# Performance work log

Measured on AMD Instinct MI355X. Metric: run time of the kernel, lower is better.

The kernel has to match this reference:

```python
import jax, jax.numpy as jnp
import numpy as np

N = 100000      # nodes
E = 1600000     # directed edges
F_IN = 128      # num_node_features
H = 256         # hidden_dim
OUT = 128       # output_dim
G = 2048        # number of graphs in batch
EPS = 1e-5      # BatchNorm eps


def setup_inputs() -> dict:
    key = jax.random.key(0)
    ks = jax.random.split(key, 8)
    x = jax.random.normal(ks[0], (N, F_IN), jnp.float32)
    row = jax.random.randint(ks[1], (E,), 0, N, dtype=jnp.int32)
    col = jax.random.randint(ks[2], (E,), 0, N, dtype=jnp.int32)
    batch = jnp.sort(jax.random.randint(ks[3], (N,), 0, G, dtype=jnp.int32))

    def lin(k, fi, fo):
        return (jax.random.normal(k, (fi, fo), jnp.float32) / np.sqrt(fi)).astype(jnp.float32)

    return {
        "x": x, "row": row, "col": col, "batch": batch,
        "W1": lin(ks[4], F_IN, H), "b1": jnp.zeros((H,), jnp.float32),
        "g1": jnp.ones((H,), jnp.float32), "be1": jnp.zeros((H,), jnp.float32),
        "W2": lin(ks[5], H, H), "b2": jnp.zeros((H,), jnp.float32),
        "g2": jnp.ones((H,), jnp.float32), "be2": jnp.zeros((H,), jnp.float32),
        "W3": lin(ks[6], H, OUT), "b3": jnp.zeros((OUT,), jnp.float32),
        "g3": jnp.ones((OUT,), jnp.float32), "be3": jnp.zeros((OUT,), jnp.float32),
    }


def gcn_conv(x, W, b, row, col):
    # PyG GCNConv: add self-loops, symmetric deg normalization, then scatter-add.
    h = x @ W                                              # [N, F_out]
    deg = jnp.ones((N,), x.dtype).at[col].add(jnp.ones((E,), x.dtype))  # +1 for self-loop
    dinv = jax.lax.rsqrt(deg)                              # deg >= 1, safe
    norm = dinv[row] * dinv[col]                           # [E]
    agg = jnp.zeros_like(h).at[col].add(h[row] * norm[:, None])
    agg = agg + h * (dinv * dinv)[:, None]                 # self-loop messages
    return agg + b


def batchnorm(x, g, b):
    # training-mode batch statistics (running stats at init are 0/1 anyway)
    m = x.mean(axis=0)
    v = x.var(axis=0)
    return g * (x - m) * jax.lax.rsqrt(v + EPS) + b


def reference(x, row, col, batch, W1, b1, g1, be1, W2, b2, g2, be2, W3, b3, g3, be3):
    h = jax.nn.relu(batchnorm(gcn_conv(x, W1, b1, row, col), g1, be1))
    h = jax.nn.relu(batchnorm(gcn_conv(h, W2, b2, row, col), g2, be2))
    h = batchnorm(gcn_conv(h, W3, b3, row, col), g3, be3)
    # global_mean_pool over graphs
    sums = jax.ops.segment_sum(h, batch, num_segments=G)   # [G, OUT]
    cnt = jax.ops.segment_sum(jnp.ones((N,), h.dtype), batch, num_segments=G)
    return sums / jnp.maximum(cnt, 1.0)[:, None]
```

## Files before the change

### kernel.cpp

```cpp
#include <hip/hip_runtime.h>

#define NN 100000
#define EE 1600000
#define GG 2048
#define EPSB 1e-5f
#define MP 100096
#define MBLK (MP / 128)
#define NB 782
#define CAP 2560

typedef unsigned short u16;
typedef unsigned long long u64;
typedef __attribute__((ext_vector_type(8))) short short8;
typedef __attribute__((ext_vector_type(4))) float f32x4;

struct alignas(4)  u16x2 { u16 v[2]; };
struct alignas(8)  u16x4 { u16 v[4]; };
struct alignas(16) u16x8 { u16 v[8]; };

__device__ __forceinline__ float b2f(u16 u) { return __uint_as_float(((unsigned)u) << 16); }
__device__ __forceinline__ u16 f2b(float f) {
    unsigned u = __float_as_uint(f);
    return (u16)((u + 0x7FFF + ((u >> 16) & 1)) >> 16);
}
__device__ __forceinline__ void gload16(const void* g, void* l) {
    __builtin_amdgcn_global_load_lds((const __attribute__((address_space(1))) void*)g,
                                     (__attribute__((address_space(3))) void*)l, 16, 0, 0);
}


__global__ void bucketA_kernel(const int* __restrict__ row, const int* __restrict__ col,
                               int* __restrict__ bcur, u64* __restrict__ bkt) {
    int e = blockIdx.x * 256 + threadIdx.x;
    if (e < EE) {
        int c = col[e], r = row[e];
        int b = c >> 7;
        int p = atomicAdd(&bcur[b * 16], 1);
        if (p < CAP) bkt[(size_t)b * CAP + p] = ((u64)r << 32) | (unsigned)c;
    }
}

__global__ void bucketB_kernel(const u64* __restrict__ bkt, const int* __restrict__ bcur,
                               int* __restrict__ pfx, int* __restrict__ rcnt,
                               float* __restrict__ dinv, int* __restrict__ btot) {
    int b = blockIdx.x, t = threadIdx.x;
    __shared__ int lcnt[128];
    __shared__ int sp[128];
    if (t < 128) lcnt[t] = 0;
    __syncthreads();
    int tot = bcur[b * 16];
    if (tot > CAP) tot = CAP;
    const u64* B = bkt + (size_t)b * CAP;
    for (int i = t; i < tot; i += 256) atomicAdd(&lcnt[(int)(B[i] & 127)], 1);
    __syncthreads();
    int n0 = b << 7;
    int pc = 0;
    if (t < 128) {
        int c = lcnt[t];
        if (n0 + t < NN) dinv[n0 + t] = rsqrtf((float)(c + 1));
        rcnt[b * 128 + t] = c;
        pc = (c + 7) & ~7;
        sp[t] = pc;
    }
    __syncthreads();
    for (int o = 1; o < 128; o <<= 1) {
        int u = (t >= o && t < 128) ? sp[t - o] : 0;
        __syncthreads();
        if (t < 128) sp[t] += u;
        __syncthreads();
    }
    if (t < 128) pfx[b * 128 + t] = sp[t] - pc;
    if (t == 127) btot[b] = sp[127];
}

__global__ void scanT_kernel(int* __restrict__ btot, float* __restrict__ dinv,
                             int* __restrict__ colptr) {
    __shared__ int sh[1024];
    int t = threadIdx.x;
    int v = (t < NB) ? btot[t] : 0;
    sh[t] = v;
    __syncthreads();
    for (int o = 1; o < 1024; o <<= 1) {
        int u = (t >= o) ? sh[t - o] : 0;
        __syncthreads();
        sh[t] += u;
        __syncthreads();
    }
    if (t < NB) btot[t] = sh[t] - v;
    if (t == NB - 1) colptr[NN] = sh[t];
    if (t == 0) dinv[NN] = 0.f;
}

__global__ void bucketC_kernel(const u64* __restrict__ bkt, const int* __restrict__ bcur,
                               const int* __restrict__ pfx, const int* __restrict__ rcnt,
                               const int* __restrict__ btot, int* __restrict__ colptr,
                               int* __restrict__ srcs) {
    int b = blockIdx.x, t = threadIdx.x;
    int n0 = b << 7;
    __shared__ int cur[128];
    int base = btot[b];
    if (t < 128) {
        int st = base + pfx[b * 128 + t];
        cur[t] = st;
        if (n0 + t < NN) colptr[n0 + t] = st;
    }
    __syncthreads();
    int tot = bcur[b * 16];
    if (tot > CAP) tot = CAP;
    const u64* B = bkt + (size_t)b * CAP;
    for (int i = t; i < tot; i += 256) {
        u64 v = B[i];
        int c = (int)(v & 127);
        int r = (int)(v >> 32);
        int p = atomicAdd(&cur[c], 1);
        srcs[p] = r;
    }
    __syncthreads();
    if (t < 128) {
        int rc = rcnt[b * 128 + t];
        int pc = (rc + 7) & ~7;
        int st = base + pfx[b * 128 + t];
        for (int i = rc; i < pc; ++i) srcs[st + i] = NN;
    }
}


__global__ void xcast_kernel(const float* __restrict__ x, u16* __restrict__ xb) {
    int idx = blockIdx.x * 256 + threadIdx.x;
    if (idx < NN * 32) {
        float4 v = ((const float4*)x)[idx];
        u16x4 o = {{f2b(v.x), f2b(v.y), f2b(v.z), f2b(v.w)}};
        ((u16x4*)xb)[idx] = o;
    }
}

__global__ void wcast_kernel(const float* __restrict__ W1, const float* __restrict__ W2,
                             const float* __restrict__ W3, u16* __restrict__ Wt1,
                             u16* __restrict__ Wt2, u16* __restrict__ Wt3) {
    int idx = blockIdx.x * 256 + threadIdx.x;
    if (idx < 32768) {
        int n = idx >> 7, k = idx & 127;
        Wt1[idx] = f2b(W1[k * 256 + n]);
    } else if (idx < 98304) {
        int j = idx - 32768;
        int n = j >> 8, k = j & 255;
        Wt2[j] = f2b(W2[k * 256 + n]);
    } else if (idx < 131072) {
        int j = idx - 98304;
        int n = j >> 8, k = j & 255;
        Wt3[j] = f2b(W3[k * 128 + n]);
    }
}


template <int F, bool TR>
__global__ void agg_kernel(const u16* __restrict__ X, u16* __restrict__ out,
                           const int* __restrict__ colptr, const int* __restrict__ srcs,
                           const float* __restrict__ dinv,
                           const float* __restrict__ sc, const float* __restrict__ shf) {
    constexpr int VE = F / 64;
    int node = blockIdx.x * 4 + (threadIdx.x >> 6);
    if (node >= NN) return;
    int l = threadIdx.x & 63;
    int f0 = l * VE;
    float s_[VE], t_[VE];
    if (TR) {
#pragma unroll
        for (int j = 0; j < VE; ++j) { s_[j] = sc[f0 + j]; t_[j] = shf[f0 + j]; }
    }
    float acc[VE] = {};
    int beg = colptr[node], end = colptr[node + 1];

    auto fetch = [&](int s, u16* u) {
        if (VE == 4) *(u16x4*)u = *(const u16x4*)(X + (size_t)s * F + f0);
        else         *(u16x2*)u = *(const u16x2*)(X + (size_t)s * F + f0);
    };
    auto accum = [&](const u16* u, float w) {
#pragma unroll
        for (int j = 0; j < VE; ++j) {
            float v = b2f(u[j]);
            if (TR) v = fmaxf(fmaf(s_[j], v, t_[j]), 0.f);
            acc[j] = fmaf(w, v, acc[j]);
        }
    };

    for (int e0 = beg; e0 < end; e0 += 64) {
        int take = end - e0;
        if (take > 64) take = 64;
        int sv = (l < take) ? srcs[e0 + l] : NN;
        float wv = dinv[sv];
        for (int j = 0; j < take; j += 8) {
            int s[8];
            float w[8];
            u16 u[8][VE];
#pragma unroll
            for (int q = 0; q < 8; ++q) {
                s[q] = __shfl(sv, j + q);
                w[q] = __shfl(wv, j + q);
            }
#pragma unroll
            for (int q = 0; q < 8; ++q) fetch(s[q], u[q]);
#pragma unroll
            for (int q = 0; q < 8; ++q) accum(u[q], w[q]);
        }
    }
    float di = dinv[node];
    u16 us[VE];
    fetch(node, us);
    accum(us, di);
    if (VE == 4) {
        u16x4 o = {{f2b(di * acc[0]), f2b(di * acc[1]), f2b(di * acc[2]), f2b(di * acc[3])}};
        *(u16x4*)(out + (size_t)node * F + f0) = o;
    } else {
        u16x2 o = {{f2b(di * acc[0]), f2b(di * acc[1])}};
        *(u16x2*)(out + (size_t)node * F + f0) = o;
    }
}


template <bool STATS, bool FUSEA>
__global__ __launch_bounds__(256) void gemm_kernel(const u16* __restrict__ A,
                                                   const u16* __restrict__ Wt,
                                                   u16* __restrict__ C,
                                                   int Kdim, int Nout,
                                                   float* __restrict__ gs,
                                                   const float* __restrict__ sc,
                                                   const float* __restrict__ shf) {
    __shared__ u16 As[128 * 64];
    __shared__ u16 Bs[128 * 64];
    __shared__ float sbuf[2][128];
    const int tid = threadIdx.x;
    const int w = tid >> 6, l = tid & 63;
    const int row0 = blockIdx.x * 128;
    const int col0 = blockIdx.y * 128;
    const int srow = w * 32 + (l >> 3);
    const int skel = (l & 7) * 8;
    const u16* Asrc = A + (size_t)(row0 + srow) * Kdim + skel;
    const u16* Bsrc = Wt + (size_t)(col0 + srow) * Kdim + skel;
    u16* AsBase = &As[w * 2048];
    u16* BsBase = &Bs[w * 2048];
    const int wr = (w >> 1) * 64, wc = (w & 1) * 64;
    f32x4 acc[4][4] = {};
    if (STATS && tid < 128) { sbuf[0][tid] = 0.f; sbuf[1][tid] = 0.f; }

    for (int k0 = 0; k0 < Kdim; k0 += 64) {
        if (FUSEA) {
            float4 sa0 = *(const float4*)&sc[k0 + skel];
            float4 sa1 = *(const float4*)&sc[k0 + skel + 4];
            float4 ta0 = *(const float4*)&shf[k0 + skel];
            float4 ta1 = *(const float4*)&shf[k0 + skel + 4];
            float sA[8] = {sa0.x, sa0.y, sa0.z, sa0.w, sa1.x, sa1.y, sa1.z, sa1.w};
            float tA[8] = {ta0.x, ta0.y, ta0.z, ta0.w, ta1.x, ta1.y, ta1.z, ta1.w};
#pragma unroll
            for (int j = 0; j < 4; ++j) {
                u16x8 av = *(const u16x8*)(Asrc + (size_t)(j * 8) * Kdim + k0);
                u16x8 o;
#pragma unroll
                for (int i = 0; i < 8; ++i)
                    o.v[i] = f2b(fmaxf(fmaf(sA[i], b2f(av.v[i]), tA[i]), 0.f));
                *(u16x8*)&As[(w * 32 + j * 8 + (l >> 3)) * 64 + skel] = o;
            }
        } else {
#pragma unroll
            for (int j = 0; j < 4; ++j)
                gload16(Asrc + (size_t)(j * 8) * Kdim + k0, AsBase + j * 512);
        }
#pragma unroll
        for (int j = 0; j < 4; ++j)
            gload16(Bsrc + (size_t)(j * 8) * Kdim + k0, BsBase + j * 512);
        __syncthreads();
#pragma unroll
        for (int ks = 0; ks < 2; ++ks) {
            short8 a[4], b[4];
#pragma unroll
            for (int mi = 0; mi < 4; ++mi)
                a[mi] = *(const short8*)&As[(wr + mi * 16 + (l & 15)) * 64 + ks * 32 + (l >> 4) * 8];
#pragma unroll
            for (int ni = 0; ni < 4; ++ni)
                b[ni] = *(const short8*)&Bs[(wc + ni * 16 + (l & 15)) * 64 + ks * 32 + (l >> 4) * 8];
#pragma unroll
            for (int mi = 0; mi < 4; ++mi)
#pragma unroll
                for (int ni = 0; ni < 4; ++ni)
                    acc[mi][ni] = __builtin_amdgcn_mfma_f32_16x16x32_bf16(a[mi], b[ni], acc[mi][ni], 0, 0, 0);
        }
        __syncthreads();
    }
    const int cr = (l >> 4) * 4, cc = l & 15;
#pragma unroll
    for (int mi = 0; mi < 4; ++mi) {
#pragma unroll
        for (int j = 0; j < 4; ++j) {
            int r = row0 + wr + mi * 16 + cr + j;
#pragma unroll
            for (int ni = 0; ni < 4; ++ni)
                C[(size_t)r * Nout + col0 + wc + ni * 16 + cc] = f2b(acc[mi][ni][j]);
        }
    }
    if (STATS) {
#pragma unroll
        for (int ni = 0; ni < 4; ++ni) {
            float s = 0.f, q = 0.f;
#pragma unroll
            for (int mi = 0; mi < 4; ++mi)
#pragma unroll
                for (int jj = 0; jj < 4; ++jj) {
                    float v = acc[mi][ni][jj];
                    s += v;
                    q += v * v;
                }
            s += __shfl_xor(s, 16); s += __shfl_xor(s, 32);
            q += __shfl_xor(q, 16); q += __shfl_xor(q, 32);
            if (l < 16) {
                atomicAdd(&sbuf[0][wc + ni * 16 + l], s);
                atomicAdd(&sbuf[1][wc + ni * 16 + l], q);
            }
        }
        __syncthreads();
        if (tid < 128) {
            size_t base = (size_t)(blockIdx.y * gridDim.x + blockIdx.x) * 256;
            gs[base + tid] = sbuf[0][tid];
            gs[base + 128 + tid] = sbuf[1][tid];
        }
    }
}

__global__ void statreduce_kernel(const float* __restrict__ gs, float* __restrict__ sums, int F) {
    int which = blockIdx.x;
    int by = blockIdx.y;
    int c = threadIdx.x;
    float s = 0.f;
    for (int bx = 0; bx < MBLK; ++bx)
        s += gs[(size_t)(by * MBLK + bx) * 256 + which * 128 + c];
    sums[which * F + by * 128 + c] = s;
}


__global__ void stats_kernel(const u16* __restrict__ Z, int F, float* __restrict__ sums) {
    int f = threadIdx.x;
    float s = 0.f, q = 0.f;
    for (int r = blockIdx.x; r < NN; r += gridDim.x) {
        float v = b2f(Z[(size_t)r * F + f]);
        s += v;
        q += v * v;
    }
    atomicAdd(&sums[f], s);
    atomicAdd(&sums[F + f], q);
}

__global__ void finalize_kernel(const float* __restrict__ sums, int F,
                                const float* __restrict__ g, const float* __restrict__ be,
                                float* __restrict__ sc, float* __restrict__ shf) {
    int f = threadIdx.x;
    if (f < F) {
        float m = sums[f] * (1.f / NN);
        float v = sums[F + f] * (1.f / NN) - m * m;
        float s = g[f] * rsqrtf(v + EPSB);
        sc[f] = s;
        shf[f] = be[f] - m * s;
    }
}


__global__ void pool_kernel(const u16* __restrict__ Z, const int* __restrict__ batch,
                            const float* __restrict__ sc, const float* __restrict__ shf,
                            float* __restrict__ out) {
    int gph = blockIdx.x;
    int f = threadIdx.x;
    __shared__ int sb, se;
    if (f == 0) {
        int lo = 0, hi = NN;
        while (lo < hi) { int mid = (lo + hi) >> 1; if (batch[mid] < gph) lo = mid + 1; else hi = mid; }
        sb = lo;
        hi = NN;
        while (lo < hi) { int mid = (lo + hi) >> 1; if (batch[mid] < gph + 1) lo = mid + 1; else hi = mid; }
        se = lo;
    }
    __syncthreads();
    int beg = sb, end = se;
    float acc = 0.f;
    for (int r = beg; r < end; ++r) acc += b2f(Z[(size_t)r * 128 + f]);
    float res = 0.f;
    int c = end - beg;
    if (c > 0) res = fmaf(sc[f], acc / (float)c, shf[f]);
    out[(size_t)gph * 128 + f] = res;
}


extern "C" void kernel_launch(void* const* d_in, const int* in_sizes, int n_in,
                              void* d_out, int out_size, void* d_ws, size_t ws_size,
                              hipStream_t stream) {
    const float* x     = (const float*)d_in[0];
    const int*   row   = (const int*)d_in[1];
    const int*   col   = (const int*)d_in[2];
    const int*   batch = (const int*)d_in[3];
    const float* W1 = (const float*)d_in[4];
    const float* g1 = (const float*)d_in[6];
    const float* be1 = (const float*)d_in[7];
    const float* W2 = (const float*)d_in[8];
    const float* g2 = (const float*)d_in[10];
    const float* be2 = (const float*)d_in[11];
    const float* W3 = (const float*)d_in[12];
    const float* g3 = (const float*)d_in[14];
    const float* be3 = (const float*)d_in[15];
    float* out = (float*)d_out;

    char* ws = (char*)d_ws;
    size_t off = 0;
    auto alloc = [&](size_t bytes) { size_t o = off; off += (bytes + 255) & ~255ULL; return o; };
    u16*   bufA   = (u16*)  (ws + alloc((size_t)MP * 256 * 2));
    u16*   bufB   = (u16*)  (ws + alloc((size_t)MP * 256 * 2));
    u16*   xb     = (u16*)  (ws + alloc((size_t)MP * 128 * 2));
    u16*   Wt1    = (u16*)  (ws + alloc(128 * 256 * 2));
    u16*   Wt2    = (u16*)  (ws + alloc(256 * 256 * 2));
    u16*   Wt3    = (u16*)  (ws + alloc(256 * 128 * 2));
    int*   colptr = (int*)  (ws + alloc((size_t)(NN + 16) * 4));
    float* dinv   = (float*)(ws + alloc((size_t)(NN + 16) * 4));
    int*   srcs   = (int*)  (ws + alloc((size_t)(EE + 8 * NN) * 4));
    u64*   bkt    = (u64*)  (ws + alloc((size_t)NB * CAP * 8));
    int*   bcur   = (int*)  (ws + alloc((size_t)NB * 16 * 4));
    int*   pfx    = (int*)  (ws + alloc((size_t)NB * 128 * 4));
    int*   rcnt   = (int*)  (ws + alloc((size_t)NB * 128 * 4));
    int*   btot   = (int*)  (ws + alloc(1024 * 4));
    float* stats  = (float*)(ws + alloc(6 * 256 * 4));
    float* scbuf  = (float*)(ws + alloc(6 * 256 * 4));
    float* gs     = (float*)(ws + alloc((size_t)MBLK * 2 * 256 * 4));

    hipMemsetAsync(bcur, 0, (size_t)NB * 16 * 4, stream);
    hipMemsetAsync(stats, 0, 6 * 256 * 4, stream);
    hipMemsetAsync((char*)bufA + (size_t)NN * 256, 0, (size_t)(MP - NN) * 256, stream);
    hipMemsetAsync((char*)bufA + (size_t)NN * 512, 0, (size_t)(MP - NN) * 512, stream);
    hipMemsetAsync((char*)xb + (size_t)NN * 256, 0, (size_t)(MP - NN) * 256, stream);

    bucketA_kernel<<<(EE + 255) / 256, 256, 0, stream>>>(row, col, bcur, bkt);
    bucketB_kernel<<<NB, 256, 0, stream>>>(bkt, bcur, pfx, rcnt, dinv, btot);
    scanT_kernel<<<1, 1024, 0, stream>>>(btot, dinv, colptr);
    bucketC_kernel<<<NB, 256, 0, stream>>>(bkt, bcur, pfx, rcnt, btot, colptr, srcs);

    xcast_kernel<<<(NN * 32 + 255) / 256, 256, 0, stream>>>(x, xb);
    wcast_kernel<<<512, 256, 0, stream>>>(W1, W2, W3, Wt1, Wt2, Wt3);

    const int aggBlocks = (NN + 3) / 4;

    agg_kernel<128, false><<<aggBlocks, 256, 0, stream>>>(xb, bufA, colptr, srcs, dinv, nullptr, nullptr);
    gemm_kernel<true, false><<<dim3(MBLK, 2), 256, 0, stream>>>(bufA, Wt1, bufB, 128, 256, gs, nullptr, nullptr);
    statreduce_kernel<<<dim3(2, 2), 128, 0, stream>>>(gs, stats + 0, 256);
    finalize_kernel<<<1, 256, 0, stream>>>(stats + 0, 256, g1, be1, scbuf + 0, scbuf + 256);

    agg_kernel<256, true><<<aggBlocks, 256, 0, stream>>>(bufB, bufA, colptr, srcs, dinv, scbuf + 0, scbuf + 256);
    gemm_kernel<true, false><<<dim3(MBLK, 2), 256, 0, stream>>>(bufA, Wt2, bufB, 256, 256, gs, nullptr, nullptr);
    statreduce_kernel<<<dim3(2, 2), 128, 0, stream>>>(gs, stats + 512, 256);
    finalize_kernel<<<1, 256, 0, stream>>>(stats + 512, 256, g2, be2, scbuf + 512, scbuf + 768);

    gemm_kernel<false, true><<<dim3(MBLK, 1), 256, 0, stream>>>(bufB, Wt3, bufA, 256, 128, gs, scbuf + 512, scbuf + 768);
    agg_kernel<128, false><<<aggBlocks, 256, 0, stream>>>(bufA, xb, colptr, srcs, dinv, nullptr, nullptr);
    stats_kernel<<<512, 128, 0, stream>>>(xb, 128, stats + 1024);
    finalize_kernel<<<1, 256, 0, stream>>>(stats + 1024, 128, g3, be3, scbuf + 1024, scbuf + 1280);

    pool_kernel<<<GG, 128, 0, stream>>>(xb, batch, scbuf + 1024, scbuf + 1280, out);
}
```

Measured before the change: 611.4 us.

## Repack aggregation to 16-byte lanes, pack edge buckets, fuse BN stats into pooling

The aggregation kernel now gives each lane 8 bf16 features, loaded as one 16-byte access, and uses subwave groups of 16 or 32 lanes per node. Gathers are double-buffered so the next batch of neighbour rows is fetched while the current one accumulates. Edge buckets pack source and local column into a 32-bit word instead of 64 bits, halving bucket traffic. The separate final BatchNorm stats pass is folded into a pooling pass that also writes per-graph sums, and a small kernel applies the affine transform afterwards. The packing assumes the source index fits in 25 bits, and gathers that are not multiples of 8 rely on the padded sentinel entries.

```diff
diff --git a/kernel.cpp b/kernel.cpp
--- a/kernel.cpp
+++ b/kernel.cpp
@@ -10,9 +10,9 @@
 #define CAP 2560
 
 typedef unsigned short u16;
-typedef unsigned long long u64;
 typedef __attribute__((ext_vector_type(8))) short short8;
 typedef __attribute__((ext_vector_type(4))) float f32x4;
+typedef __attribute__((ext_vector_type(2))) float f32x2;
 
 struct alignas(4)  u16x2 { u16 v[2]; };
 struct alignas(8)  u16x4 { u16 v[4]; };
@@ -30,17 +30,17 @@
 
 
 __global__ void bucketA_kernel(const int* __restrict__ row, const int* __restrict__ col,
-                               int* __restrict__ bcur, u64* __restrict__ bkt) {
+                               int* __restrict__ bcur, unsigned* __restrict__ bkt) {
     int e = blockIdx.x * 256 + threadIdx.x;
     if (e < EE) {
         int c = col[e], r = row[e];
         int b = c >> 7;
         int p = atomicAdd(&bcur[b * 16], 1);
-        if (p < CAP) bkt[(size_t)b * CAP + p] = ((u64)r << 32) | (unsigned)c;
-    }
-}
-
-__global__ void bucketB_kernel(const u64* __restrict__ bkt, const int* __restrict__ bcur,
+        if (p < CAP) bkt[(size_t)b * CAP + p] = ((unsigned)r << 7) | (unsigned)(c & 127);
+    }
+}
+
+__global__ void bucketB_kernel(const unsigned* __restrict__ bkt, const int* __restrict__ bcur,
                                int* __restrict__ pfx, int* __restrict__ rcnt,
                                float* __restrict__ dinv, int* __restrict__ btot) {
     int b = blockIdx.x, t = threadIdx.x;
@@ -50,8 +50,8 @@
     __syncthreads();
     int tot = bcur[b * 16];
     if (tot > CAP) tot = CAP;
-    const u64* B = bkt + (size_t)b * CAP;
-    for (int i = t; i < tot; i += 256) atomicAdd(&lcnt[(int)(B[i] & 127)], 1);
+    const unsigned* B = bkt + (size_t)b * CAP;
+    for (int i = t; i < tot; i += 256) atomicAdd(&lcnt[(int)(B[i] & 127u)], 1);
     __syncthreads();
     int n0 = b << 7;
     int pc = 0;
@@ -91,7 +91,7 @@
     if (t == 0) dinv[NN] = 0.f;
 }
 
-__global__ void bucketC_kernel(const u64* __restrict__ bkt, const int* __restrict__ bcur,
+__global__ void bucketC_kernel(const unsigned* __restrict__ bkt, const int* __restrict__ bcur,
                                const int* __restrict__ pfx, const int* __restrict__ rcnt,
                                const int* __restrict__ btot, int* __restrict__ colptr,
                                int* __restrict__ srcs) {
@@ -107,11 +107,11 @@
     __syncthreads();
     int tot = bcur[b * 16];
     if (tot > CAP) tot = CAP;
-    const u64* B = bkt + (size_t)b * CAP;
+    const unsigned* B = bkt + (size_t)b * CAP;
     for (int i = t; i < tot; i += 256) {
-        u64 v = B[i];
-        int c = (int)(v & 127);
-        int r = (int)(v >> 32);
+        unsigned v = B[i];
+        int c = (int)(v & 127u);
+        int r = (int)(v >> 7);
         int p = atomicAdd(&cur[c], 1);
         srcs[p] = r;
     }
@@ -153,68 +153,86 @@
 }
 
 
-template <int F, bool TR>
+template <int XS, bool TR>
 __global__ void agg_kernel(const u16* __restrict__ X, u16* __restrict__ out,
                            const int* __restrict__ colptr, const int* __restrict__ srcs,
                            const float* __restrict__ dinv,
                            const float* __restrict__ sc, const float* __restrict__ shf) {
-    constexpr int VE = F / 64;
-    int node = blockIdx.x * 4 + (threadIdx.x >> 6);
+    constexpr int GROUP = XS / 8;
+    constexpr int NPB = 256 / GROUP;
+    int node = blockIdx.x * NPB + threadIdx.x / GROUP;
     if (node >= NN) return;
-    int l = threadIdx.x & 63;
-    int f0 = l * VE;
-    float s_[VE], t_[VE];
+    int l = threadIdx.x & (GROUP - 1);
+    int f0 = l * 8;
+    const u16* Xf = X + f0;
+    f32x2 s2[4], t2[4];
     if (TR) {
-#pragma unroll
-        for (int j = 0; j < VE; ++j) { s_[j] = sc[f0 + j]; t_[j] = shf[f0 + j]; }
-    }
-    float acc[VE] = {};
+        float4 sa = *(const float4*)&sc[f0], sb = *(const float4*)&sc[f0 + 4];
+        float4 ta = *(const float4*)&shf[f0], tb = *(const float4*)&shf[f0 + 4];
+        s2[0] = f32x2{sa.x, sa.y}; s2[1] = f32x2{sa.z, sa.w};
+        s2[2] = f32x2{sb.x, sb.y}; s2[3] = f32x2{sb.z, sb.w};
+        t2[0] = f32x2{ta.x, ta.y}; t2[1] = f32x2{ta.z, ta.w};
+        t2[2] = f32x2{tb.x, tb.y}; t2[3] = f32x2{tb.z, tb.w};
+    }
+    f32x2 acc[4] = {};
+    const f32x2 z2 = {0.f, 0.f};
+
+    auto accum = [&](const u16x8& u, float w) {
+        f32x2 w2 = {w, w};
+        const unsigned* p = (const unsigned*)&u;
+#pragma unroll
+        for (int j = 0; j < 4; ++j) {
+            unsigned q = p[j];
+            f32x2 v = {__uint_as_float(q << 16), __uint_as_float(q & 0xffff0000u)};
+            if (TR) {
+                v = __builtin_elementwise_fma(s2[j], v, t2[j]);
+                v = __builtin_elementwise_max(v, z2);
+            }
+            acc[j] = __builtin_elementwise_fma(w2, v, acc[j]);
+        }
+    };
+
+#define FETCHB(kk, buf) do { _Pragma("unroll") \
+    for (int q = 0; q < 8; ++q) { \
+        int s_ = __shfl(sv, (kk) * 8 + q, GROUP); \
+        buf[q] = *(const u16x8*)(Xf + (size_t)s_ * XS); } } while (0)
+#define ACCB(kk, buf) do { _Pragma("unroll") \
+    for (int q = 0; q < 8; ++q) { \
+        float w_ = __shfl(wv, (kk) * 8 + q, GROUP); \
+        accum(buf[q], w_); } } while (0)
+
     int beg = colptr[node], end = colptr[node + 1];
-
-    auto fetch = [&](int s, u16* u) {
-        if (VE == 4) *(u16x4*)u = *(const u16x4*)(X + (size_t)s * F + f0);
-        else         *(u16x2*)u = *(const u16x2*)(X + (size_t)s * F + f0);
-    };
-    auto accum = [&](const u16* u, float w) {
-#pragma unroll
-        for (int j = 0; j < VE; ++j) {
-            float v = b2f(u[j]);
-            if (TR) v = fmaxf(fmaf(s_[j], v, t_[j]), 0.f);
-            acc[j] = fmaf(w, v, acc[j]);
-        }
-    };
-
-    for (int e0 = beg; e0 < end; e0 += 64) {
+    for (int e0 = beg; e0 < end; e0 += GROUP) {
         int take = end - e0;
-        if (take > 64) take = 64;
+        if (take > GROUP) take = GROUP;
         int sv = (l < take) ? srcs[e0 + l] : NN;
         float wv = dinv[sv];
-        for (int j = 0; j < take; j += 8) {
-            int s[8];
-            float w[8];
-            u16 u[8][VE];
-#pragma unroll
-            for (int q = 0; q < 8; ++q) {
-                s[q] = __shfl(sv, j + q);
-                w[q] = __shfl(wv, j + q);
-            }
-#pragma unroll
-            for (int q = 0; q < 8; ++q) fetch(s[q], u[q]);
-#pragma unroll
-            for (int q = 0; q < 8; ++q) accum(u[q], w[q]);
-        }
-    }
+        int b = take >> 3;
+        u16x8 A_[8], B_[8];
+        FETCHB(0, A_);
+        int k = 1;
+        for (; k + 1 < b; k += 2) {
+            FETCHB(k, B_); ACCB(k - 1, A_);
+            FETCHB(k + 1, A_); ACCB(k, B_);
+        }
+        if (k < b) { FETCHB(k, B_); ACCB(k - 1, A_); ACCB(k, B_); }
+        else ACCB(k - 1, A_);
+    }
+#undef FETCHB
+#undef ACCB
+
     float di = dinv[node];
-    u16 us[VE];
-    fetch(node, us);
+    u16x8 us = *(const u16x8*)(Xf + (size_t)node * XS);
     accum(us, di);
-    if (VE == 4) {
-        u16x4 o = {{f2b(di * acc[0]), f2b(di * acc[1]), f2b(di * acc[2]), f2b(di * acc[3])}};
-        *(u16x4*)(out + (size_t)node * F + f0) = o;
-    } else {
-        u16x2 o = {{f2b(di * acc[0]), f2b(di * acc[1])}};
-        *(u16x2*)(out + (size_t)node * F + f0) = o;
-    }
+    f32x2 d2 = {di, di};
+    u16x8 o;
+#pragma unroll
+    for (int j = 0; j < 4; ++j) {
+        f32x2 r = acc[j] * d2;
+        o.v[2 * j] = f2b(r[0]);
+        o.v[2 * j + 1] = f2b(r[1]);
+    }
+    *(u16x8*)(out + (size_t)node * XS + f0) = o;
 }
 
 
@@ -335,19 +353,6 @@
     sums[which * F + by * 128 + c] = s;
 }
 
-
-__global__ void stats_kernel(const u16* __restrict__ Z, int F, float* __restrict__ sums) {
-    int f = threadIdx.x;
-    float s = 0.f, q = 0.f;
-    for (int r = blockIdx.x; r < NN; r += gridDim.x) {
-        float v = b2f(Z[(size_t)r * F + f]);
-        s += v;
-        q += v * v;
-    }
-    atomicAdd(&sums[f], s);
-    atomicAdd(&sums[F + f], q);
-}
-
 __global__ void finalize_kernel(const float* __restrict__ sums, int F,
                                 const float* __restrict__ g, const float* __restrict__ be,
                                 float* __restrict__ sc, float* __restrict__ shf) {
@@ -362,9 +367,9 @@
 }
 
 
-__global__ void pool_kernel(const u16* __restrict__ Z, const int* __restrict__ batch,
-                            const float* __restrict__ sc, const float* __restrict__ shf,
-                            float* __restrict__ out) {
+__global__ void poolstats_kernel(const u16* __restrict__ Z, const int* __restrict__ batch,
+                                 float* __restrict__ gsum, int* __restrict__ gcnt,
+                                 float* __restrict__ sums) {
     int gph = blockIdx.x;
     int f = threadIdx.x;
     __shared__ int sb, se;
@@ -378,12 +383,27 @@
     }
     __syncthreads();
     int beg = sb, end = se;
-    float acc = 0.f;
-    for (int r = beg; r < end; ++r) acc += b2f(Z[(size_t)r * 128 + f]);
-    float res = 0.f;
-    int c = end - beg;
-    if (c > 0) res = fmaf(sc[f], acc / (float)c, shf[f]);
-    out[(size_t)gph * 128 + f] = res;
+    float acc = 0.f, qq = 0.f;
+    for (int r = beg; r < end; ++r) {
+        float v = b2f(Z[(size_t)r * 128 + f]);
+        acc += v;
+        qq += v * v;
+    }
+    gsum[(size_t)gph * 128 + f] = acc;
+    if (f == 0) gcnt[gph] = end - beg;
+    atomicAdd(&sums[f], acc);
+    atomicAdd(&sums[128 + f], qq);
+}
+
+__global__ void poolout_kernel(const float* __restrict__ gsum, const int* __restrict__ gcnt,
+                               const float* __restrict__ sc, const float* __restrict__ shf,
+                               float* __restrict__ out) {
+    int i = blockIdx.x * 256 + threadIdx.x;
+    if (i < GG * 128) {
+        int g = i >> 7, f = i & 127;
+        int c = gcnt[g];
+        out[i] = (c > 0) ? fmaf(sc[f], gsum[i] / (float)c, shf[f]) : 0.f;
+    }
 }
 
 
@@ -417,7 +437,7 @@
     int*   colptr = (int*)  (ws + alloc((size_t)(NN + 16) * 4));
     float* dinv   = (float*)(ws + alloc((size_t)(NN + 16) * 4));
     int*   srcs   = (int*)  (ws + alloc((size_t)(EE + 8 * NN) * 4));
-    u64*   bkt    = (u64*)  (ws + alloc((size_t)NB * CAP * 8));
+    unsigned* bkt = (unsigned*)(ws + alloc((size_t)NB * CAP * 4));
     int*   bcur   = (int*)  (ws + alloc((size_t)NB * 16 * 4));
     int*   pfx    = (int*)  (ws + alloc((size_t)NB * 128 * 4));
     int*   rcnt   = (int*)  (ws + alloc((size_t)NB * 128 * 4));
@@ -425,6 +445,8 @@
     float* stats  = (float*)(ws + alloc(6 * 256 * 4));
     float* scbuf  = (float*)(ws + alloc(6 * 256 * 4));
     float* gs     = (float*)(ws + alloc((size_t)MBLK * 2 * 256 * 4));
+    float* gsum   = (float*)(ws + alloc((size_t)GG * 128 * 4));
+    int*   gcnt   = (int*)  (ws + alloc((size_t)GG * 4));
 
     hipMemsetAsync(bcur, 0, (size_t)NB * 16 * 4, stream);
     hipMemsetAsync(stats, 0, 6 * 256 * 4, stream);
@@ -440,22 +462,19 @@
     xcast_kernel<<<(NN * 32 + 255) / 256, 256, 0, stream>>>(x, xb);
     wcast_kernel<<<512, 256, 0, stream>>>(W1, W2, W3, Wt1, Wt2, Wt3);
 
-    const int aggBlocks = (NN + 3) / 4;
-
-    agg_kernel<128, false><<<aggBlocks, 256, 0, stream>>>(xb, bufA, colptr, srcs, dinv, nullptr, nullptr);
+    agg_kernel<128, false><<<NN / 16, 256, 0, stream>>>(xb, bufA, colptr, srcs, dinv, nullptr, nullptr);
     gemm_kernel<true, false><<<dim3(MBLK, 2), 256, 0, stream>>>(bufA, Wt1, bufB, 128, 256, gs, nullptr, nullptr);
     statreduce_kernel<<<dim3(2, 2), 128, 0, stream>>>(gs, stats + 0, 256);
     finalize_kernel<<<1, 256, 0, stream>>>(stats + 0, 256, g1, be1, scbuf + 0, scbuf + 256);
 
-    agg_kernel<256, true><<<aggBlocks, 256, 0, stream>>>(bufB, bufA, colptr, srcs, dinv, scbuf + 0, scbuf + 256);
+    agg_kernel<256, true><<<NN / 8, 256, 0, stream>>>(bufB, bufA, colptr, srcs, dinv, scbuf + 0, scbuf + 256);
     gemm_kernel<true, false><<<dim3(MBLK, 2), 256, 0, stream>>>(bufA, Wt2, bufB, 256, 256, gs, nullptr, nullptr);
     statreduce_kernel<<<dim3(2, 2), 128, 0, stream>>>(gs, stats + 512, 256);
     finalize_kernel<<<1, 256, 0, stream>>>(stats + 512, 256, g2, be2, scbuf + 512, scbuf + 768);
 
     gemm_kernel<false, true><<<dim3(MBLK, 1), 256, 0, stream>>>(bufB, Wt3, bufA, 256, 128, gs, scbuf + 512, scbuf + 768);
-    agg_kernel<128, false><<<aggBlocks, 256, 0, stream>>>(bufA, xb, colptr, srcs, dinv, nullptr, nullptr);
-    stats_kernel<<<512, 128, 0, stream>>>(xb, 128, stats + 1024);
+    agg_kernel<128, false><<<NN / 16, 256, 0, stream>>>(bufA, xb, colptr, srcs, dinv, nullptr, nullptr);
+    poolstats_kernel<<<GG, 128, 0, stream>>>(xb, batch, gsum, gcnt, stats + 1024);
     finalize_kernel<<<1, 256, 0, stream>>>(stats + 1024, 128, g3, be3, scbuf + 1024, scbuf + 1280);
-
-    pool_kernel<<<GG, 128, 0, stream>>>(xb, batch, scbuf + 1024, scbuf + 1280, out);
-}
+    poolout_kernel<<<(GG * 128 + 255) / 256, 256, 0, stream>>>(gsum, gcnt, scbuf + 1024, scbuf + 1280, out);
+}
```

Result: slower. 807.0 us (+32.0%).

## Fuse setup kernels, drop global scan, merge stats into pooling pass

Applied to the files above, without the earlier changes.

Replaces the memsets with one init kernel and merges the bucket count and scatter kernels. It drops the global prefix scan by giving each bucket a fixed CAPP slot with per-node begin and end arrays. Bucket entries are packed into 32 bits, and the x and W cast kernels are fused. It folds the layer-3 statistics pass into the pooling read and fuses statreduce with finalize. The goal is fewer launches and one less full pass over the final activations, at the cost of a sparser srcs layout and a fixed per-bucket capacity assumption.

```diff
diff --git a/kernel.cpp b/kernel.cpp
--- a/kernel.cpp
+++ b/kernel.cpp
@@ -8,9 +8,9 @@
 #define MBLK (MP / 128)
 #define NB 782
 #define CAP 2560
+#define CAPP 3584
 
 typedef unsigned short u16;
-typedef unsigned long long u64;
 typedef __attribute__((ext_vector_type(8))) short short8;
 typedef __attribute__((ext_vector_type(4))) float f32x4;
 
@@ -29,37 +29,55 @@
 }
 
 
+#define ZB0 (NB * 16)
+#define ZB1 (ZB0 + 256)
+#define ZB2 (ZB1 + 1)
+#define ZB3 (ZB2 + (MP - NN) * 64)
+#define ZB4 (ZB3 + (MP - NN) * 128)
+
+__global__ void init_kernel(unsigned* __restrict__ bcur, unsigned* __restrict__ p3stats,
+                            unsigned* __restrict__ dinvNN, unsigned* __restrict__ padA128,
+                            unsigned* __restrict__ padA256) {
+    int i = blockIdx.x * 256 + threadIdx.x;
+    if (i < ZB0) bcur[i] = 0u;
+    else if (i < ZB1) p3stats[i - ZB0] = 0u;
+    else if (i < ZB2) dinvNN[0] = 0u;
+    else if (i < ZB3) padA128[i - ZB2] = 0u;
+    else if (i < ZB4) padA256[i - ZB3] = 0u;
+}
+
+
 __global__ void bucketA_kernel(const int* __restrict__ row, const int* __restrict__ col,
-                               int* __restrict__ bcur, u64* __restrict__ bkt) {
+                               int* __restrict__ bcur, unsigned* __restrict__ bkt) {
     int e = blockIdx.x * 256 + threadIdx.x;
     if (e < EE) {
         int c = col[e], r = row[e];
         int b = c >> 7;
         int p = atomicAdd(&bcur[b * 16], 1);
-        if (p < CAP) bkt[(size_t)b * CAP + p] = ((u64)r << 32) | (unsigned)c;
-    }
-}
-
-__global__ void bucketB_kernel(const u64* __restrict__ bkt, const int* __restrict__ bcur,
-                               int* __restrict__ pfx, int* __restrict__ rcnt,
-                               float* __restrict__ dinv, int* __restrict__ btot) {
+        if (p < CAP) bkt[(size_t)b * CAP + p] = ((unsigned)r << 7) | (unsigned)(c & 127);
+    }
+}
+
+__global__ void bucketBC_kernel(const unsigned* __restrict__ bkt, const int* __restrict__ bcur,
+                                int* __restrict__ begs, int* __restrict__ ends,
+                                float* __restrict__ dinv, int* __restrict__ srcs) {
     int b = blockIdx.x, t = threadIdx.x;
     __shared__ int lcnt[128];
     __shared__ int sp[128];
+    __shared__ int cur[128];
     if (t < 128) lcnt[t] = 0;
     __syncthreads();
     int tot = bcur[b * 16];
     if (tot > CAP) tot = CAP;
-    const u64* B = bkt + (size_t)b * CAP;
-    for (int i = t; i < tot; i += 256) atomicAdd(&lcnt[(int)(B[i] & 127)], 1);
+    const unsigned* B = bkt + (size_t)b * CAP;
+    for (int i = t; i < tot; i += 256) atomicAdd(&lcnt[(int)(B[i] & 127u)], 1);
     __syncthreads();
     int n0 = b << 7;
     int pc = 0;
     if (t < 128) {
-        int c = lcnt[t];
-        if (n0 + t < NN) dinv[n0 + t] = rsqrtf((float)(c + 1));
-        rcnt[b * 128 + t] = c;
-        pc = (c + 7) & ~7;
+        int rc = lcnt[t];
+        if (n0 + t < NN) dinv[n0 + t] = rsqrtf((float)(rc + 1));
+        pc = (rc + 7) & ~7;
         sp[t] = pc;
     }
     __syncthreads();
@@ -69,94 +87,58 @@
         if (t < 128) sp[t] += u;
         __syncthreads();
     }
-    if (t < 128) pfx[b * 128 + t] = sp[t] - pc;
-    if (t == 127) btot[b] = sp[127];
-}
-
-__global__ void scanT_kernel(int* __restrict__ btot, float* __restrict__ dinv,
-                             int* __restrict__ colptr) {
-    __shared__ int sh[1024];
-    int t = threadIdx.x;
-    int v = (t < NB) ? btot[t] : 0;
-    sh[t] = v;
-    __syncthreads();
-    for (int o = 1; o < 1024; o <<= 1) {
-        int u = (t >= o) ? sh[t - o] : 0;
-        __syncthreads();
-        sh[t] += u;
-        __syncthreads();
-    }
-    if (t < NB) btot[t] = sh[t] - v;
-    if (t == NB - 1) colptr[NN] = sh[t];
-    if (t == 0) dinv[NN] = 0.f;
-}
-
-__global__ void bucketC_kernel(const u64* __restrict__ bkt, const int* __restrict__ bcur,
-                               const int* __restrict__ pfx, const int* __restrict__ rcnt,
-                               const int* __restrict__ btot, int* __restrict__ colptr,
-                               int* __restrict__ srcs) {
-    int b = blockIdx.x, t = threadIdx.x;
-    int n0 = b << 7;
-    __shared__ int cur[128];
-    int base = btot[b];
+    int base = b * CAPP;
     if (t < 128) {
-        int st = base + pfx[b * 128 + t];
+        int st = base + sp[t] - pc;
         cur[t] = st;
-        if (n0 + t < NN) colptr[n0 + t] = st;
-    }
-    __syncthreads();
-    int tot = bcur[b * 16];
-    if (tot > CAP) tot = CAP;
-    const u64* B = bkt + (size_t)b * CAP;
+        if (n0 + t < NN) { begs[n0 + t] = st; ends[n0 + t] = st + pc; }
+    }
+    __syncthreads();
     for (int i = t; i < tot; i += 256) {
-        u64 v = B[i];
-        int c = (int)(v & 127);
-        int r = (int)(v >> 32);
-        int p = atomicAdd(&cur[c], 1);
-        srcs[p] = r;
-    }
-    __syncthreads();
-    if (t < 128) {
-        int rc = rcnt[b * 128 + t];
-        int pc = (rc + 7) & ~7;
-        int st = base + pfx[b * 128 + t];
-        for (int i = rc; i < pc; ++i) srcs[st + i] = NN;
-    }
-}
-
-
-__global__ void xcast_kernel(const float* __restrict__ x, u16* __restrict__ xb) {
+        unsigned v = B[i];
+        int p = atomicAdd(&cur[(int)(v & 127u)], 1);
+        srcs[p] = (int)(v >> 7);
+    }
+    __syncthreads();
+    if (t < 128 && n0 + t < NN) {
+        int st = cur[t];
+        int en = base + sp[t];
+        for (int i = st; i < en; ++i) srcs[i] = NN;
+    }
+}
+
+
+__global__ void xwcast_kernel(const float* __restrict__ x, u16* __restrict__ xb,
+                              const float* __restrict__ W1, const float* __restrict__ W2,
+                              const float* __restrict__ W3, u16* __restrict__ Wt1,
+                              u16* __restrict__ Wt2, u16* __restrict__ Wt3) {
     int idx = blockIdx.x * 256 + threadIdx.x;
     if (idx < NN * 32) {
         float4 v = ((const float4*)x)[idx];
         u16x4 o = {{f2b(v.x), f2b(v.y), f2b(v.z), f2b(v.w)}};
         ((u16x4*)xb)[idx] = o;
-    }
-}
-
-__global__ void wcast_kernel(const float* __restrict__ W1, const float* __restrict__ W2,
-                             const float* __restrict__ W3, u16* __restrict__ Wt1,
-                             u16* __restrict__ Wt2, u16* __restrict__ Wt3) {
-    int idx = blockIdx.x * 256 + threadIdx.x;
-    if (idx < 32768) {
-        int n = idx >> 7, k = idx & 127;
-        Wt1[idx] = f2b(W1[k * 256 + n]);
-    } else if (idx < 98304) {
-        int j = idx - 32768;
-        int n = j >> 8, k = j & 255;
-        Wt2[j] = f2b(W2[k * 256 + n]);
-    } else if (idx < 131072) {
-        int j = idx - 98304;
-        int n = j >> 8, k = j & 255;
-        Wt3[j] = f2b(W3[k * 128 + n]);
+        return;
+    }
+    int j = idx - NN * 32;
+    if (j < 32768) {
+        int n = j >> 7, k = j & 127;
+        Wt1[j] = f2b(W1[k * 256 + n]);
+    } else if (j < 98304) {
+        int jj = j - 32768;
+        int n = jj >> 8, k = jj & 255;
+        Wt2[jj] = f2b(W2[k * 256 + n]);
+    } else if (j < 131072) {
+        int jj = j - 98304;
+        int n = jj >> 8, k = jj & 255;
+        Wt3[jj] = f2b(W3[k * 128 + n]);
     }
 }
 
 
 template <int F, bool TR>
 __global__ void agg_kernel(const u16* __restrict__ X, u16* __restrict__ out,
-                           const int* __restrict__ colptr, const int* __restrict__ srcs,
-                           const float* __restrict__ dinv,
+                           const int* __restrict__ begs, const int* __restrict__ ends,
+                           const int* __restrict__ srcs, const float* __restrict__ dinv,
                            const float* __restrict__ sc, const float* __restrict__ shf) {
     constexpr int VE = F / 64;
     int node = blockIdx.x * 4 + (threadIdx.x >> 6);
@@ -169,7 +151,7 @@
         for (int j = 0; j < VE; ++j) { s_[j] = sc[f0 + j]; t_[j] = shf[f0 + j]; }
     }
     float acc[VE] = {};
-    int beg = colptr[node], end = colptr[node + 1];
+    int beg = begs[node], end = ends[node];
 
     auto fetch = [&](int s, u16* u) {
         if (VE == 4) *(u16x4*)u = *(const u16x4*)(X + (size_t)s * F + f0);
@@ -325,27 +307,24 @@
     }
 }
 
-__global__ void statreduce_kernel(const float* __restrict__ gs, float* __restrict__ sums, int F) {
-    int which = blockIdx.x;
-    int by = blockIdx.y;
-    int c = threadIdx.x;
-    float s = 0.f;
-    for (int bx = 0; bx < MBLK; ++bx)
-        s += gs[(size_t)(by * MBLK + bx) * 256 + which * 128 + c];
-    sums[which * F + by * 128 + c] = s;
-}
-
-
-__global__ void stats_kernel(const u16* __restrict__ Z, int F, float* __restrict__ sums) {
-    int f = threadIdx.x;
+
+__global__ void statfin_kernel(const float* __restrict__ gs,
+                               const float* __restrict__ g, const float* __restrict__ be,
+                               float* __restrict__ sc, float* __restrict__ shf) {
+    int by = blockIdx.x;
+    int t = threadIdx.x;
+    const float* base = gs + (size_t)by * MBLK * 256;
     float s = 0.f, q = 0.f;
-    for (int r = blockIdx.x; r < NN; r += gridDim.x) {
-        float v = b2f(Z[(size_t)r * F + f]);
-        s += v;
-        q += v * v;
-    }
-    atomicAdd(&sums[f], s);
-    atomicAdd(&sums[F + f], q);
+    for (int bx = 0; bx < MBLK; ++bx) {
+        s += base[(size_t)bx * 256 + t];
+        q += base[(size_t)bx * 256 + 128 + t];
+    }
+    int c = by * 128 + t;
+    float m = s * (1.f / NN);
+    float v = q * (1.f / NN) - m * m;
+    float scv = g[c] * rsqrtf(v + EPSB);
+    sc[c] = scv;
+    shf[c] = be[c] - m * scv;
 }
 
 __global__ void finalize_kernel(const float* __restrict__ sums, int F,
@@ -362,9 +341,9 @@
 }
 
 
-__global__ void pool_kernel(const u16* __restrict__ Z, const int* __restrict__ batch,
-                            const float* __restrict__ sc, const float* __restrict__ shf,
-                            float* __restrict__ out) {
+__global__ void poolstats_kernel(const u16* __restrict__ Z, const int* __restrict__ batch,
+                                 float* __restrict__ gsum, int* __restrict__ gcnt,
+                                 float* __restrict__ sums) {
     int gph = blockIdx.x;
     int f = threadIdx.x;
     __shared__ int sb, se;
@@ -378,12 +357,27 @@
     }
     __syncthreads();
     int beg = sb, end = se;
-    float acc = 0.f;
-    for (int r = beg; r < end; ++r) acc += b2f(Z[(size_t)r * 128 + f]);
-    float res = 0.f;
-    int c = end - beg;
-    if (c > 0) res = fmaf(sc[f], acc / (float)c, shf[f]);
-    out[(size_t)gph * 128 + f] = res;
+    float acc = 0.f, qq = 0.f;
+    for (int r = beg; r < end; ++r) {
+        float v = b2f(Z[(size_t)r * 128 + f]);
+        acc += v;
+        qq += v * v;
+    }
+    gsum[(size_t)gph * 128 + f] = acc;
+    if (f == 0) gcnt[gph] = end - beg;
+    atomicAdd(&sums[f], acc);
+    atomicAdd(&sums[128 + f], qq);
+}
+
+__global__ void poolout_kernel(const float* __restrict__ gsum, const int* __restrict__ gcnt,
+                               const float* __restrict__ sc, const float* __restrict__ shf,
+                               float* __restrict__ out) {
+    int i = blockIdx.x * 256 + threadIdx.x;
+    if (i < GG * 128) {
+        int g = i >> 7, f = i & 127;
+        int c = gcnt[g];
+        out[i] = (c > 0) ? fmaf(sc[f], gsum[i] / (float)c, shf[f]) : 0.f;
+    }
 }
 
 
@@ -414,48 +408,41 @@
     u16*   Wt1    = (u16*)  (ws + alloc(128 * 256 * 2));
     u16*   Wt2    = (u16*)  (ws + alloc(256 * 256 * 2));
     u16*   Wt3    = (u16*)  (ws + alloc(256 * 128 * 2));
-    int*   colptr = (int*)  (ws + alloc((size_t)(NN + 16) * 4));
+    int*   begs   = (int*)  (ws + alloc((size_t)(NN + 16) * 4));
+    int*   ends   = (int*)  (ws + alloc((size_t)(NN + 16) * 4));
     float* dinv   = (float*)(ws + alloc((size_t)(NN + 16) * 4));
-    int*   srcs   = (int*)  (ws + alloc((size_t)(EE + 8 * NN) * 4));
-    u64*   bkt    = (u64*)  (ws + alloc((size_t)NB * CAP * 8));
+    int*   srcs   = (int*)  (ws + alloc((size_t)NB * CAPP * 4));
+    unsigned* bkt = (unsigned*)(ws + alloc((size_t)NB * CAP * 4));
     int*   bcur   = (int*)  (ws + alloc((size_t)NB * 16 * 4));
-    int*   pfx    = (int*)  (ws + alloc((size_t)NB * 128 * 4));
-    int*   rcnt   = (int*)  (ws + alloc((size_t)NB * 128 * 4));
-    int*   btot   = (int*)  (ws + alloc(1024 * 4));
-    float* stats  = (float*)(ws + alloc(6 * 256 * 4));
+    float* p3stats= (float*)(ws + alloc(256 * 4));
     float* scbuf  = (float*)(ws + alloc(6 * 256 * 4));
     float* gs     = (float*)(ws + alloc((size_t)MBLK * 2 * 256 * 4));
-
-    hipMemsetAsync(bcur, 0, (size_t)NB * 16 * 4, stream);
-    hipMemsetAsync(stats, 0, 6 * 256 * 4, stream);
-    hipMemsetAsync((char*)bufA + (size_t)NN * 256, 0, (size_t)(MP - NN) * 256, stream);
-    hipMemsetAsync((char*)bufA + (size_t)NN * 512, 0, (size_t)(MP - NN) * 512, stream);
-    hipMemsetAsync((char*)xb + (size_t)NN * 256, 0, (size_t)(MP - NN) * 256, stream);
+    float* gsum   = (float*)(ws + alloc((size_t)GG * 128 * 4));
+    int*   gcnt   = (int*)  (ws + alloc((size_t)GG * 4));
+
+    init_kernel<<<(ZB4 + 255) / 256, 256, 0, stream>>>(
+        (unsigned*)bcur, (unsigned*)p3stats, (unsigned*)&dinv[NN],
+        (unsigned*)(bufA + (size_t)NN * 128), (unsigned*)(bufA + (size_t)NN * 256));
 
     bucketA_kernel<<<(EE + 255) / 256, 256, 0, stream>>>(row, col, bcur, bkt);
-    bucketB_kernel<<<NB, 256, 0, stream>>>(bkt, bcur, pfx, rcnt, dinv, btot);
-    scanT_kernel<<<1, 1024, 0, stream>>>(btot, dinv, colptr);
-    bucketC_kernel<<<NB, 256, 0, stream>>>(bkt, bcur, pfx, rcnt, btot, colptr, srcs);
-
-    xcast_kernel<<<(NN * 32 + 255) / 256, 256, 0, stream>>>(x, xb);
-    wcast_kernel<<<512, 256, 0, stream>>>(W1, W2, W3, Wt1, Wt2, Wt3);
+    bucketBC_kernel<<<NB, 256, 0, stream>>>(bkt, bcur, begs, ends, dinv, srcs);
+
+    xwcast_kernel<<<(NN * 32 + 131072 + 255) / 256, 256, 0, stream>>>(
+        x, xb, W1, W2, W3, Wt1, Wt2, Wt3);
 
     const int aggBlocks = (NN + 3) / 4;
 
-    agg_kernel<128, false><<<aggBlocks, 256, 0, stream>>>(xb, bufA, colptr, srcs, dinv, nullptr, nullptr);
+    agg_kernel<128, false><<<aggBlocks, 256, 0, stream>>>(xb, bufA, begs, ends, srcs, dinv, nullptr, nullptr);
     gemm_kernel<true, false><<<dim3(MBLK, 2), 256, 0, stream>>>(bufA, Wt1, bufB, 128, 256, gs, nullptr, nullptr);
-    statreduce_kernel<<<dim3(2, 2), 128, 0, stream>>>(gs, stats + 0, 256);
-    finalize_kernel<<<1, 256, 0, stream>>>(stats + 0, 256, g1, be1, scbuf + 0, scbuf + 256);
-
-    agg_kernel<256, true><<<aggBlocks, 256, 0, stream>>>(bufB, bufA, colptr, srcs, dinv, scbuf + 0, scbuf + 256);
+    statfin_kernel<<<2, 128, 0, stream>>>(gs, g1, be1, scbuf + 0, scbuf + 256);
+
+    agg_kernel<256, true><<<aggBlocks, 256, 0, stream>>>(bufB, bufA, begs, ends, srcs, dinv, scbuf + 0, scbuf + 256);
     gemm_kernel<true, false><<<dim3(MBLK, 2), 256, 0, stream>>>(bufA, Wt2, bufB, 256, 256, gs, nullptr, nullptr);
-    statreduce_kernel<<<dim3(2, 2), 128, 0, stream>>>(gs, stats + 512, 256);
-    finalize_kernel<<<1, 256, 0, stream>>>(stats + 512, 256, g2, be2, scbuf + 512, scbuf + 768);
+    statfin_kernel<<<2, 128, 0, stream>>>(gs, g2, be2, scbuf + 512, scbuf + 768);
 
     gemm_kernel<false, true><<<dim3(MBLK, 1), 256, 0, stream>>>(bufB, Wt3, bufA, 256, 128, gs, scbuf + 512, scbuf + 768);
-    agg_kernel<128, false><<<aggBlocks, 256, 0, stream>>>(bufA, xb, colptr, srcs, dinv, nullptr, nullptr);
-    stats_kernel<<<512, 128, 0, stream>>>(xb, 128, stats + 1024);
-    finalize_kernel<<<1, 256, 0, stream>>>(stats + 1024, 128, g3, be3, scbuf + 1024, scbuf + 1280);
-
-    pool_kernel<<<GG, 128, 0, stream>>>(xb, batch, scbuf + 1024, scbuf + 1280, out);
-}
+    agg_kernel<128, false><<<aggBlocks, 256, 0, stream>>>(bufA, xb, begs, ends, srcs, dinv, nullptr, nullptr);
+    poolstats_kernel<<<GG, 128, 0, stream>>>(xb, batch, gsum, gcnt, p3stats);
+    finalize_kernel<<<1, 256, 0, stream>>>(p3stats, 128, g3, be3, scbuf + 1024, scbuf + 1280);
+    poolout_kernel<<<(GG * 128 + 255) / 256, 256, 0, stream>>>(gsum, gcnt, scbuf + 1024, scbuf + 1280, out);
+}
```

Result: slower. 730.4 us (+19.5%).
